# Optimization experiments

Measured on AMD Instinct MI355X. Metric: run time of the kernel, lower is better.

## Reference

```python
import jax, jax.numpy as jnp
import numpy as np

N = 50000
NEG_SLOPE = 0.2


def gat_conv(x, src, dst, W, al, ar, b, res=None, activation=None):
    # x: [N, F_in]; W: [F_in, H*D]; al, ar: [H, D]; b: [H*D]
    H, D = al.shape
    h = (x @ W).reshape(-1, H, D)                      # [N, H, D]
    el = jnp.sum(h * al, axis=-1)                      # [N, H]
    er = jnp.sum(h * ar, axis=-1)                      # [N, H]
    e = jax.nn.leaky_relu(el[src] + er[dst], NEG_SLOPE)  # [E, H]
    # edge softmax grouped by destination node
    m = jax.ops.segment_max(e, dst, num_segments=N)    # [N, H]
    ex = jnp.exp(e - m[dst])
    s = jax.ops.segment_sum(ex, dst, num_segments=N)   # [N, H]
    alpha = ex / s[dst]                                # [E, H]
    msg = h[src] * alpha[..., None]                    # [E, H, D]
    out = jax.ops.segment_sum(msg, dst, num_segments=N)  # [N, H, D]
    if res is not None:
        if res is True:  # identity residual (F_in == H*D)
            out = out + x.reshape(-1, H, D)
        else:            # projected residual, res: [F_in, H*D]
            out = out + (x @ res).reshape(-1, H, D)
    out = out + b.reshape(1, H, D)
    if activation is not None:
        out = activation(out)
    return out


def setup_inputs() -> dict:
    key = jax.random.key(0)
    ks = jax.random.split(key, 16)
    E = 800000
    IN, HID, CLS, H = 256, 64, 32, 2
    x = jax.random.normal(ks[0], (N, IN), dtype=jnp.float32)
    edge_src = jax.random.randint(ks[1], (E,), 0, N, dtype=jnp.int32)
    edge_dst = jax.random.randint(ks[2], (E,), 0, N, dtype=jnp.int32)

    def lin(k, fi, fo):
        return jax.random.normal(k, (fi, fo), dtype=jnp.float32) * (1.0 / np.sqrt(fi))

    W0 = lin(ks[3], IN, H * HID)
    al0 = jax.random.normal(ks[4], (H, HID), dtype=jnp.float32) * 0.1
    ar0 = jax.random.normal(ks[5], (H, HID), dtype=jnp.float32) * 0.1
    b0 = jnp.zeros((H * HID,), dtype=jnp.float32)
    W1 = lin(ks[6], H * HID, H * HID)
    al1 = jax.random.normal(ks[7], (H, HID), dtype=jnp.float32) * 0.1
    ar1 = jax.random.normal(ks[8], (H, HID), dtype=jnp.float32) * 0.1
    b1 = jnp.zeros((H * HID,), dtype=jnp.float32)
    W2 = lin(ks[9], H * HID, H * CLS)
    al2 = jax.random.normal(ks[10], (H, CLS), dtype=jnp.float32) * 0.1
    ar2 = jax.random.normal(ks[11], (H, CLS), dtype=jnp.float32) * 0.1
    b2 = jnp.zeros((H * CLS,), dtype=jnp.float32)
    Wres2 = lin(ks[12], H * HID, H * CLS)
    return {"x": x, "edge_src": edge_src, "edge_dst": edge_dst,
            "W0": W0, "al0": al0, "ar0": ar0, "b0": b0,
            "W1": W1, "al1": al1, "ar1": ar1, "b1": b1,
            "W2": W2, "al2": al2, "ar2": ar2, "b2": b2,
            "Wres2": Wres2}


def reference(x, edge_src, edge_dst, W0, al0, ar0, b0, W1, al1, ar1, b1,
              W2, al2, ar2, b2, Wres2):
    elu = jax.nn.elu
    h = gat_conv(x, edge_src, edge_dst, W0, al0, ar0, b0,
                 res=None, activation=elu)
    h = h.reshape(h.shape[0], -1)  # flatten heads: [N, H*D]
    h = gat_conv(h, edge_src, edge_dst, W1, al1, ar1, b1,
                 res=True, activation=elu)  # identity residual
    h = h.reshape(h.shape[0], -1)
    h = gat_conv(h, edge_src, edge_dst, W2, al2, ar2, b2,
                 res=Wres2, activation=None)  # [N, H, CLS]
    logits = h.mean(axis=1)  # mean over heads -> [N, CLS]
    return logits
```

## Files before the change

kernel.cpp:

```cpp
#include <hip/hip_runtime.h>
#include <math.h>


typedef unsigned int uint;
typedef unsigned short ushort;
typedef __attribute__((ext_vector_type(8))) short bf16x8;
typedef __attribute__((ext_vector_type(4))) float f32x4;

#define NBK 196
#define BCAP 4608

__device__ inline uint f2bf(float f) {
    uint u = __float_as_uint(f);
    return (u + 0x7fffu + ((u >> 16) & 1u)) >> 16;
}

__device__ inline uint4 pack8(float4 a, float4 b) {
    return make_uint4(f2bf(a.x) | (f2bf(a.y) << 16), f2bf(a.z) | (f2bf(a.w) << 16),
                      f2bf(b.x) | (f2bf(b.y) << 16), f2bf(b.z) | (f2bf(b.w) << 16));
}

__global__ __launch_bounds__(256) void buildA_k(
    const int* __restrict__ src, const int* __restrict__ dst, int E,
    int* __restrict__ bcur, uint* __restrict__ bdata, int nba,
    const float* __restrict__ W0, const float* __restrict__ W1,
    const float* __restrict__ W2, const float* __restrict__ Wr,
    ushort* __restrict__ Wt0, ushort* __restrict__ Wt1,
    ushort* __restrict__ Wt2cat) {
    __shared__ int lhist[NBK];
    __shared__ int gbase[NBK];
    const int t = threadIdx.x;
    if ((int)blockIdx.x >= nba) {
        int wb = blockIdx.x - nba;
        if (wb < 128) {
            int i = wb * 256 + t;
            int n = i >> 8, k = i & 255;
            Wt0[n * 256 + k] = (ushort)f2bf(W0[k * 128 + n]);
        } else if (wb < 192) {
            int i = (wb - 128) * 256 + t;
            int n = i >> 7, k = i & 127;
            Wt1[n * 128 + k] = (ushort)f2bf(W1[k * 128 + n]);
        } else if (wb < 224) {
            int i = (wb - 192) * 256 + t;
            int n = i >> 7, k = i & 127;
            Wt2cat[n * 128 + k] = (ushort)f2bf(W2[k * 64 + n]);
        } else {
            int i = (wb - 224) * 256 + t;
            int n = i >> 7, k = i & 127;
            Wt2cat[(64 + n) * 128 + k] = (ushort)f2bf(Wr[k * 64 + n]);
        }
        return;
    }
    for (int i = t; i < NBK; i += 256) lhist[i] = 0;
    __syncthreads();
    const int e0 = blockIdx.x * 2048 + t * 8;
    uint payload[8], meta[8];
#pragma unroll
    for (int i = 0; i < 8; ++i) {
        int e = e0 + i;
        if (e < E) {
            int s = src[e], d = dst[e];
            int b = d >> 8;
            int r = atomicAdd(&lhist[b], 1);
            payload[i] = ((uint)s << 8) | (uint)(d & 255);
            meta[i] = ((uint)b << 16) | (uint)r;
        } else {
            meta[i] = 0xffffffffu;
        }
    }
    __syncthreads();
    for (int i = t; i < NBK; i += 256) {
        int c = lhist[i];
        gbase[i] = c ? atomicAdd(&bcur[i], c) : 0;
    }
    __syncthreads();
#pragma unroll
    for (int i = 0; i < 8; ++i) {
        if (meta[i] != 0xffffffffu) {
            int b = meta[i] >> 16;
            int pos = gbase[b] + (int)(meta[i] & 0xffffu);
            if (pos < BCAP) bdata[(size_t)b * BCAP + pos] = payload[i];
        }
    }
}

__global__ __launch_bounds__(256) void bscan_k(const int* __restrict__ bcur,
                                               int* __restrict__ bbase) {
    __shared__ int sm[256];
    int t = threadIdx.x;
    int v = (t < NBK) ? min(bcur[t], BCAP) : 0;
    sm[t] = v;
    __syncthreads();
    for (int o = 1; o < 256; o <<= 1) {
        int add = (t >= o) ? sm[t - o] : 0;
        __syncthreads();
        sm[t] += add;
        __syncthreads();
    }
    if (t < NBK) bbase[t] = sm[t] - v;
}

__global__ __launch_bounds__(256) void bucketB_k(
    const uint* __restrict__ bdata, const int* __restrict__ bcur,
    const int* __restrict__ bbase, int* __restrict__ deg,
    int* __restrict__ offs, int* __restrict__ ssrc, int n,
    int* __restrict__ meta, int* __restrict__ nl0, int* __restrict__ nl1,
    int* __restrict__ nl2) {
    __shared__ int lhist[256], lofs[256], lcur[256], stmp[256];
    __shared__ int lc[3], lb[3];
    const int b = blockIdx.x, t = threadIdx.x;
    const int cnt = min(bcur[b], BCAP);
    const int gb = bbase[b];
    lhist[t] = 0;
    if (t < 3) lc[t] = 0;
    __syncthreads();
    const uint* bd = bdata + (size_t)b * BCAP;
    for (int i = t; i < cnt; i += 256)
        atomicAdd(&lhist[bd[i] & 255], 1);
    __syncthreads();
    int v = lhist[t];
    stmp[t] = v;
    __syncthreads();
    for (int o = 1; o < 256; o <<= 1) {
        int add = (t >= o) ? stmp[t - o] : 0;
        __syncthreads();
        stmp[t] += add;
        __syncthreads();
    }
    lofs[t] = stmp[t] - v;
    lcur[t] = 0;
    __syncthreads();
    int node = b * 256 + t;
    int cls = -1, r = 0;
    if (node < n) {
        deg[node] = v;
        offs[node] = gb + lofs[t];
        cls = (v <= 16) ? 0 : ((v <= 32) ? 1 : 2);
        r = atomicAdd(&lc[cls], 1);
    }
    __syncthreads();
    if (t < 3) lb[t] = lc[t] ? atomicAdd(&meta[t], lc[t]) : 0;
    __syncthreads();
    if (node < n) {
        int* nl = (cls == 0) ? nl0 : ((cls == 1) ? nl1 : nl2);
        nl[lb[cls] + r] = node;
    }
    for (int i = t; i < cnt; i += 256) {
        uint p = bd[i];
        int dl = p & 255;
        int rr = atomicAdd(&lcur[dl], 1);
        ssrc[gb + lofs[dl] + rr] = (int)(p >> 8);
    }
}

template <int K, bool L2MODE, bool AFP32>
__global__ __launch_bounds__(256) void gemm_m(
    const float* __restrict__ Af, const ushort* __restrict__ Ab,
    const ushort* __restrict__ Wt, ushort* __restrict__ Hb,
    float* __restrict__ hres, int nrows,
    const float* __restrict__ al, const float* __restrict__ ar,
    float* __restrict__ el, float* __restrict__ er) {
    constexpr int BK = 64;
    constexpr int AS = 72;
    __shared__ float smem[8448 + 256];
    ushort* As = (ushort*)smem;
    ushort* Ws = (ushort*)smem + 64 * AS;
    float* alr = smem + 8448;
    const int tid = threadIdx.x;
    const int w = tid >> 6;
    const int lane = tid & 63;
    const int l15 = lane & 15, quad = lane >> 4;
    const int row0 = blockIdx.x * 64;
    constexpr int NC = L2MODE ? 64 : 128;

    if (tid < 2 * NC) alr[tid] = (tid < NC) ? al[tid] : ar[tid - NC];

    f32x4 acc[8];
#pragma unroll
    for (int i = 0; i < 8; ++i) acc[i] = (f32x4){0.f, 0.f, 0.f, 0.f};

    for (int kt = 0; kt < K / BK; ++kt) {
        const int k0 = kt * BK;
        if (AFP32) {
#pragma unroll
            for (int t = 0; t < 4; ++t) {
                int idx = tid + t * 256;
                int r = idx >> 4, c4 = idx & 15;
                float4 v = make_float4(0.f, 0.f, 0.f, 0.f);
                if (row0 + r < nrows)
                    v = *(const float4*)&Af[(size_t)(row0 + r) * K + k0 + c4 * 4];
                ushort4 o;
                o.x = (ushort)f2bf(v.x); o.y = (ushort)f2bf(v.y);
                o.z = (ushort)f2bf(v.z); o.w = (ushort)f2bf(v.w);
                *(ushort4*)&As[r * AS + c4 * 4] = o;
            }
        } else {
#pragma unroll
            for (int t = 0; t < 2; ++t) {
                int idx = tid + t * 256;
                int r = idx >> 3, c8 = idx & 7;
                uint4 v = make_uint4(0, 0, 0, 0);
                if (row0 + r < nrows)
                    v = *(const uint4*)&Ab[(size_t)(row0 + r) * K + k0 + c8 * 8];
                *(uint4*)&As[r * AS + c8 * 8] = v;
            }
        }
#pragma unroll
        for (int t = 0; t < 4; ++t) {
            int idx = tid + t * 256;
            int n = idx >> 3, c8 = idx & 7;
            *(uint4*)&Ws[n * AS + c8 * 8] =
                *(const uint4*)&Wt[(size_t)n * K + k0 + c8 * 8];
        }
        __syncthreads();
#pragma unroll
        for (int ks = 0; ks < 2; ++ks) {
            bf16x8 af = *(const bf16x8*)&As[(w * 16 + l15) * AS + ks * 32 + quad * 8];
#pragma unroll
            for (int ct = 0; ct < 8; ++ct) {
                bf16x8 bf = *(const bf16x8*)&Ws[(ct * 16 + l15) * AS + ks * 32 + quad * 8];
                acc[ct] = __builtin_amdgcn_mfma_f32_16x16x32_bf16(af, bf, acc[ct], 0, 0, 0);
            }
        }
        __syncthreads();
    }

    float* Cs = smem;
#pragma unroll
    for (int ct = 0; ct < 8; ++ct)
#pragma unroll
        for (int r = 0; r < 4; ++r)
            Cs[(w * 16 + quad * 4 + r) * 132 + ct * 16 + l15] = acc[ct][r];
    __syncthreads();

    if (L2MODE) {
#pragma unroll
        for (int t = 0; t < 2; ++t) {
            int chunk = tid + t * 256;
            int r = chunk >> 3, c8 = chunk & 7;
            int grow = row0 + r;
            if (grow < nrows) {
                float4 v0 = *(float4*)&Cs[r * 132 + c8 * 8];
                float4 v1 = *(float4*)&Cs[r * 132 + c8 * 8 + 4];
                *(uint4*)&Hb[(size_t)grow * 64 + c8 * 8] = pack8(v0, v1);
            }
        }
#pragma unroll
        for (int t = 0; t < 4; ++t) {
            int chunk = tid + t * 256;
            int r = chunk >> 4, c4 = chunk & 15;
            int grow = row0 + r;
            if (grow < nrows)
                *(float4*)&hres[(size_t)grow * 64 + c4 * 4] =
                    *(float4*)&Cs[r * 132 + 64 + c4 * 4];
        }
    } else {
#pragma unroll
        for (int t = 0; t < 4; ++t) {
            int chunk = tid + t * 256;
            int r = chunk >> 4, c8 = chunk & 15;
            int grow = row0 + r;
            if (grow < nrows) {
                float4 v0 = *(float4*)&Cs[r * 132 + c8 * 8];
                float4 v1 = *(float4*)&Cs[r * 132 + c8 * 8 + 4];
                *(uint4*)&Hb[(size_t)grow * 128 + c8 * 8] = pack8(v0, v1);
            }
        }
    }
    {
        constexpr int HD = L2MODE ? 32 : 64;
        int r = tid >> 2, hh = (tid >> 1) & 1, iser = tid & 1;
        int grow = row0 + r;
        const float* coef = alr + iser * NC + hh * HD;
        const float* crow = Cs + r * 132 + hh * HD;
        float sum = 0.f;
#pragma unroll
        for (int i = 0; i < HD; ++i) sum += crow[i] * coef[i];
        if (grow < nrows) (iser ? er : el)[grow * 2 + hh] = sum;
    }
}

template <int D, bool MEAN_HEADS, bool RES_BF16, int LPN>
__device__ __forceinline__ void agg_group(
    int node, int lane, float2* __restrict__ wlsw,
    const int* __restrict__ ssrc, const int* __restrict__ offs,
    const int* __restrict__ deg, const ushort* __restrict__ hb,
    const float* __restrict__ el, const float* __restrict__ er,
    const float* __restrict__ bias, const void* __restrict__ res,
    float* __restrict__ out, ushort* __restrict__ outb, int act) {
    constexpr int F = 2 * D;
    constexpr int CH = F / 8;
    constexpr int ESL = LPN / CH;
    constexpr int UB = 8;
    static_assert(ESL >= 1, "LPN must cover a full row");
    const int g = lane / LPN, sl = lane % LPN;
    const bool valid = node >= 0;
    float2* wls = wlsw + g * (LPN * 2);
    int off = 0, dg = 0;
    float2 ern = make_float2(0.f, 0.f);
    if (valid) {
        off = offs[node];
        dg = deg[node];
        ern = *(const float2*)&er[node * 2];
    }
    const uint4* __restrict__ hp = (const uint4*)hb;
    const int c = sl & (CH - 1);
    const int es = sl / CH;
    const int h1 = (c >= CH / 2) ? 1 : 0;
    const float2* wbase = wls + es * 2 + h1;
    float acc[8];
#pragma unroll
    for (int i = 0; i < 8; ++i) acc[i] = 0.f;

    auto inner = [&](int cnt) {
        for (int p = 0; p < cnt; p += UB * ESL) {
            float2 mw[UB];
#pragma unroll
            for (int u = 0; u < UB; ++u) mw[u] = wbase[(p + u * ESL) * 2];
            uint4 q[UB];
#pragma unroll
            for (int u = 0; u < UB; ++u)
                q[u] = hp[(size_t)__float_as_int(mw[u].x) * CH + c];
#pragma unroll
            for (int u = 0; u < UB; ++u) {
                float wj = mw[u].y;
                acc[0] += wj * __uint_as_float(q[u].x << 16);
                acc[1] += wj * __uint_as_float(q[u].x & 0xffff0000u);
                acc[2] += wj * __uint_as_float(q[u].y << 16);
                acc[3] += wj * __uint_as_float(q[u].y & 0xffff0000u);
                acc[4] += wj * __uint_as_float(q[u].z << 16);
                acc[5] += wj * __uint_as_float(q[u].z & 0xffff0000u);
                acc[6] += wj * __uint_as_float(q[u].w << 16);
                acc[7] += wj * __uint_as_float(q[u].w & 0xffff0000u);
            }
        }
    };

    bool big = false;
    if constexpr (LPN == 64) big = (dg > 64);

    if (!big) {
        int sidx = 0;
        float a = -INFINITY, b = -INFINITY;
        if (valid && sl < dg) {
            sidx = ssrc[off + sl];
            float2 ev = *(const float2*)&el[sidx * 2];
            a = ev.x + ern.x; a = fmaxf(a, 0.2f * a);
            b = ev.y + ern.y; b = fmaxf(b, 0.2f * b);
        }
        float m0 = a, m1 = b;
#pragma unroll
        for (int o = LPN / 2; o; o >>= 1) {
            m0 = fmaxf(m0, __shfl_xor(m0, o));
            m1 = fmaxf(m1, __shfl_xor(m1, o));
        }
        float p0 = (valid && sl < dg) ? __expf(a - m0) : 0.f;
        float p1 = (valid && sl < dg) ? __expf(b - m1) : 0.f;
        float s0 = p0, s1 = p1;
#pragma unroll
        for (int o = LPN / 2; o; o >>= 1) {
            s0 += __shfl_xor(s0, o);
            s1 += __shfl_xor(s1, o);
        }
        float is0 = s0 > 0.f ? 1.f / s0 : 0.f;
        float is1 = s1 > 0.f ? 1.f / s1 : 0.f;
        wls[sl * 2 + 0] = make_float2(__int_as_float(sidx), p0 * is0);
        wls[sl * 2 + 1] = make_float2(__int_as_float(sidx), p1 * is1);
        inner(dg);
    } else if constexpr (LPN == 64) {
        float s0 = 0.f, s1 = 0.f;
        float m0 = -INFINITY, m1 = -INFINITY;
        for (int k = sl; k < dg; k += 64) {
            int sidx = ssrc[off + k];
            float2 ev = *(const float2*)&el[sidx * 2];
            float a = ev.x + ern.x; a = fmaxf(a, 0.2f * a);
            float b = ev.y + ern.y; b = fmaxf(b, 0.2f * b);
            float nm = fmaxf(m0, a);
            s0 = s0 * __expf(m0 - nm) + __expf(a - nm); m0 = nm;
            nm = fmaxf(m1, b);
            s1 = s1 * __expf(m1 - nm) + __expf(b - nm); m1 = nm;
        }
        for (int o = 32; o; o >>= 1) {
            float om = __shfl_xor(m0, o), os = __shfl_xor(s0, o);
            float nm = fmaxf(m0, om);
            s0 = (nm == -INFINITY) ? 0.f : s0 * __expf(m0 - nm) + os * __expf(om - nm);
            m0 = nm;
            om = __shfl_xor(m1, o); os = __shfl_xor(s1, o);
            nm = fmaxf(m1, om);
            s1 = (nm == -INFINITY) ? 0.f : s1 * __expf(m1 - nm) + os * __expf(om - nm);
            m1 = nm;
        }
        float is0 = s0 > 0.f ? 1.f / s0 : 0.f;
        float is1 = s1 > 0.f ? 1.f / s1 : 0.f;
        for (int cc = 0; cc < dg; cc += 64) {
            int k = cc + sl;
            int sidx = 0;
            float w0 = 0.f, w1 = 0.f;
            if (k < dg) {
                sidx = ssrc[off + k];
                float2 ev = *(const float2*)&el[sidx * 2];
                float a = ev.x + ern.x; a = fmaxf(a, 0.2f * a);
                float b = ev.y + ern.y; b = fmaxf(b, 0.2f * b);
                w0 = __expf(a - m0) * is0;
                w1 = __expf(b - m1) * is1;
            }
            wls[sl * 2 + 0] = make_float2(__int_as_float(sidx), w0);
            wls[sl * 2 + 1] = make_float2(__int_as_float(sidx), w1);
            inner(min(64, dg - cc));
        }
    }

#pragma unroll
    for (int o = CH; o < LPN; o <<= 1) {
#pragma unroll
        for (int i = 0; i < 8; ++i) acc[i] += __shfl_xor(acc[i], o);
    }
    if (!valid) return;

    const int f0 = c * 8;
    float4 b0v = *(const float4*)&bias[f0];
    float4 b1v = *(const float4*)&bias[f0 + 4];
    float vv[8] = {acc[0] + b0v.x, acc[1] + b0v.y, acc[2] + b0v.z, acc[3] + b0v.w,
                   acc[4] + b1v.x, acc[5] + b1v.y, acc[6] + b1v.z, acc[7] + b1v.w};
    if (res) {
        if (RES_BF16) {
            uint4 r = ((const uint4*)res)[(size_t)node * CH + c];
            vv[0] += __uint_as_float(r.x << 16);
            vv[1] += __uint_as_float(r.x & 0xffff0000u);
            vv[2] += __uint_as_float(r.y << 16);
            vv[3] += __uint_as_float(r.y & 0xffff0000u);
            vv[4] += __uint_as_float(r.z << 16);
            vv[5] += __uint_as_float(r.z & 0xffff0000u);
            vv[6] += __uint_as_float(r.w << 16);
            vv[7] += __uint_as_float(r.w & 0xffff0000u);
        } else {
            const float* rf = (const float*)res;
            float4 r0v = *(const float4*)&rf[(size_t)node * F + f0];
            float4 r1v = *(const float4*)&rf[(size_t)node * F + f0 + 4];
            vv[0] += r0v.x; vv[1] += r0v.y; vv[2] += r0v.z; vv[3] += r0v.w;
            vv[4] += r1v.x; vv[5] += r1v.y; vv[6] += r1v.z; vv[7] += r1v.w;
        }
    }
    if (act) {
#pragma unroll
        for (int i = 0; i < 8; ++i)
            vv[i] = vv[i] > 0.f ? vv[i] : __expf(vv[i]) - 1.f;
    }
    if (MEAN_HEADS) {
        float ov[8];
#pragma unroll
        for (int i = 0; i < 8; ++i) ov[i] = __shfl_xor(vv[i], CH / 2);
        if (es == 0 && c < CH / 2) {
            float4 u0 = make_float4(0.5f * (vv[0] + ov[0]), 0.5f * (vv[1] + ov[1]),
                                    0.5f * (vv[2] + ov[2]), 0.5f * (vv[3] + ov[3]));
            float4 u1 = make_float4(0.5f * (vv[4] + ov[4]), 0.5f * (vv[5] + ov[5]),
                                    0.5f * (vv[6] + ov[6]), 0.5f * (vv[7] + ov[7]));
            *(float4*)&out[(size_t)node * D + f0] = u0;
            *(float4*)&out[(size_t)node * D + f0 + 4] = u1;
        }
    } else if (es == 0) {
        if (out) {
            *(float4*)&out[(size_t)node * F + f0] =
                make_float4(vv[0], vv[1], vv[2], vv[3]);
            *(float4*)&out[(size_t)node * F + f0 + 4] =
                make_float4(vv[4], vv[5], vv[6], vv[7]);
        }
        if (outb) {
            *(uint4*)&outb[(size_t)node * F + f0] =
                pack8(make_float4(vv[0], vv[1], vv[2], vv[3]),
                      make_float4(vv[4], vv[5], vv[6], vv[7]));
        }
    }
}

template <int D, bool MEAN_HEADS, bool RES_BF16>
__global__ __launch_bounds__(256) void agg_c2(
    const int* __restrict__ meta, const int* __restrict__ nl0,
    const int* __restrict__ nl1, const int* __restrict__ nl2,
    const int* __restrict__ ssrc, const int* __restrict__ offs,
    const int* __restrict__ deg, const ushort* __restrict__ hb,
    const float* __restrict__ el, const float* __restrict__ er,
    const float* __restrict__ bias, const void* __restrict__ res,
    float* __restrict__ out, ushort* __restrict__ outb, int act) {
    __shared__ float2 wls_all[4][128];
    const int wid = threadIdx.x >> 6;
    const int lane = threadIdx.x & 63;
    float2* wls = wls_all[wid];
    const int c0 = meta[0], c1 = meta[1], c2 = meta[2];
    const int I0 = (c0 + 3) >> 2;
    const int I01 = I0 + ((c1 + 1) >> 1);
    const int T = I01 + c2;
    const int nW = gridDim.x * 4;
    for (int it = blockIdx.x * 4 + wid; it < T; it += nW) {
        if (it < I0) {
            int idx = it * 4 + (lane >> 4);
            int node = (idx < c0) ? nl0[idx] : -1;
            agg_group<D, MEAN_HEADS, RES_BF16, 16>(node, lane, wls, ssrc, offs,
                                                   deg, hb, el, er, bias, res,
                                                   out, outb, act);
        } else if (it < I01) {
            int idx = (it - I0) * 2 + (lane >> 5);
            int node = (idx < c1) ? nl1[idx] : -1;
            agg_group<D, MEAN_HEADS, RES_BF16, 32>(node, lane, wls, ssrc, offs,
                                                   deg, hb, el, er, bias, res,
                                                   out, outb, act);
        } else {
            int node = nl2[it - I01];
            agg_group<D, MEAN_HEADS, RES_BF16, 64>(node, lane, wls, ssrc, offs,
                                                   deg, hb, el, er, bias, res,
                                                   out, outb, act);
        }
    }
}


extern "C" void kernel_launch(void* const* d_in, const int* in_sizes, int n_in,
                              void* d_out, int out_size, void* d_ws, size_t ws_size,
                              hipStream_t stream) {
    const float* x     = (const float*)d_in[0];
    const int*   esrc  = (const int*)d_in[1];
    const int*   edst  = (const int*)d_in[2];
    const float* W0    = (const float*)d_in[3];
    const float* al0   = (const float*)d_in[4];
    const float* ar0   = (const float*)d_in[5];
    const float* b0    = (const float*)d_in[6];
    const float* W1    = (const float*)d_in[7];
    const float* al1   = (const float*)d_in[8];
    const float* ar1   = (const float*)d_in[9];
    const float* b1    = (const float*)d_in[10];
    const float* W2    = (const float*)d_in[11];
    const float* al2   = (const float*)d_in[12];
    const float* ar2   = (const float*)d_in[13];
    const float* b2    = (const float*)d_in[14];
    const float* Wres2 = (const float*)d_in[15];

    const int N = in_sizes[0] / 256;
    const int E = in_sizes[1];

    float* ws = (float*)d_ws;
    float* hres  = ws;
    float* el    = hres + (size_t)N * 64;
    float* er    = el + (size_t)N * 2;
    int* deg     = (int*)(er + (size_t)N * 2);
    int* offs    = deg + N;
    int* bcur    = offs + N;
    int* bbase   = bcur + 256;
    int* ssrc    = bbase + 256;
    uint* bdata  = (uint*)(ssrc + E);
    ushort* Hb   = (ushort*)(bdata + (size_t)NBK * BCAP);
    ushort* Ab   = Hb + (size_t)N * 128;
    ushort* Bb   = Ab + (size_t)N * 128;
    ushort* Wt0  = Bb + (size_t)N * 128;
    ushort* Wt1  = Wt0 + 128 * 256;
    ushort* Wt2c = Wt1 + 128 * 128;
    int* nl0     = (int*)(Wt2c + 128 * 128);
    int* nl1     = nl0 + N;
    int* nl2     = nl1 + N;
    int* meta    = bcur + 208;

    hipMemsetAsync(bcur, 0, 256 * sizeof(int), stream);
    const int nba = (E + 2047) / 2048;
    buildA_k<<<nba + 256, 256, 0, stream>>>(esrc, edst, E, bcur, bdata, nba,
                                            W0, W1, W2, Wres2, Wt0, Wt1, Wt2c);
    bscan_k<<<1, 256, 0, stream>>>(bcur, bbase);
    bucketB_k<<<NBK, 256, 0, stream>>>(bdata, bcur, bbase, deg, offs, ssrc, N,
                                       meta, nl0, nl1, nl2);

    int gblk = (N + 63) / 64;
    const int ablk = 2048;

    gemm_m<256, false, true><<<gblk, 256, 0, stream>>>(
        x, nullptr, Wt0, Hb, nullptr, N, al0, ar0, el, er);
    agg_c2<64, false, false><<<ablk, 256, 0, stream>>>(
        meta, nl0, nl1, nl2, ssrc, offs, deg, Hb, el, er, b0, nullptr,
        nullptr, Ab, 1);

    gemm_m<128, false, false><<<gblk, 256, 0, stream>>>(
        nullptr, Ab, Wt1, Hb, nullptr, N, al1, ar1, el, er);
    agg_c2<64, false, true><<<ablk, 256, 0, stream>>>(
        meta, nl0, nl1, nl2, ssrc, offs, deg, Hb, el, er, b1, Ab,
        nullptr, Bb, 1);

    gemm_m<128, true, false><<<gblk, 256, 0, stream>>>(
        nullptr, Bb, Wt2c, Hb, hres, N, al2, ar2, el, er);
    agg_c2<32, true, false><<<ablk, 256, 0, stream>>>(
        meta, nl0, nl1, nl2, ssrc, offs, deg, Hb, el, er, b2, hres,
        (float*)d_out, nullptr, 0);
}
```

Baseline: 276.4 us.

## Fold bucket scan into bucketB and load GEMM operands directly from global

```diff
diff --git a/kernel.cpp b/kernel.cpp
--- a/kernel.cpp
+++ b/kernel.cpp
@@ -84,36 +84,29 @@
     }
 }
 
-__global__ __launch_bounds__(256) void bscan_k(const int* __restrict__ bcur,
-                                               int* __restrict__ bbase) {
-    __shared__ int sm[256];
-    int t = threadIdx.x;
-    int v = (t < NBK) ? min(bcur[t], BCAP) : 0;
-    sm[t] = v;
-    __syncthreads();
-    for (int o = 1; o < 256; o <<= 1) {
-        int add = (t >= o) ? sm[t - o] : 0;
-        __syncthreads();
-        sm[t] += add;
-        __syncthreads();
-    }
-    if (t < NBK) bbase[t] = sm[t] - v;
-}
-
 __global__ __launch_bounds__(256) void bucketB_k(
     const uint* __restrict__ bdata, const int* __restrict__ bcur,
-    const int* __restrict__ bbase, int* __restrict__ deg,
-    int* __restrict__ offs, int* __restrict__ ssrc, int n,
-    int* __restrict__ meta, int* __restrict__ nl0, int* __restrict__ nl1,
-    int* __restrict__ nl2) {
+    int* __restrict__ deg, int* __restrict__ offs, int* __restrict__ ssrc,
+    int n, int* __restrict__ meta, int* __restrict__ nl0,
+    int* __restrict__ nl1, int* __restrict__ nl2) {
     __shared__ int lhist[256], lofs[256], lcur[256], stmp[256];
-    __shared__ int lc[3], lb[3];
+    __shared__ int lc[3], lb[3], sgb;
     const int b = blockIdx.x, t = threadIdx.x;
     const int cnt = min(bcur[b], BCAP);
-    const int gb = bbase[b];
+    int cv = (t < NBK) ? min(bcur[t], BCAP) : 0;
+    stmp[t] = cv;
     lhist[t] = 0;
     if (t < 3) lc[t] = 0;
     __syncthreads();
+    for (int o = 1; o < 256; o <<= 1) {
+        int add = (t >= o) ? stmp[t - o] : 0;
+        __syncthreads();
+        stmp[t] += add;
+        __syncthreads();
+    }
+    if (t == 0) sgb = b ? stmp[b - 1] : 0;
+    __syncthreads();
+    const int gb = sgb;
     const uint* bd = bdata + (size_t)b * BCAP;
     for (int i = t; i < cnt; i += 256)
         atomicAdd(&lhist[bd[i] & 255], 1);
@@ -160,12 +153,9 @@
     float* __restrict__ hres, int nrows,
     const float* __restrict__ al, const float* __restrict__ ar,
     float* __restrict__ el, float* __restrict__ er) {
-    constexpr int BK = 64;
-    constexpr int AS = 72;
-    __shared__ float smem[8448 + 256];
-    ushort* As = (ushort*)smem;
-    ushort* Ws = (ushort*)smem + 64 * AS;
-    float* alr = smem + 8448;
+    __shared__ float smem[64 * 132 + 256];
+    float* Cs = smem;
+    float* alr = smem + 64 * 132;
     const int tid = threadIdx.x;
     const int w = tid >> 6;
     const int lane = tid & 63;
@@ -175,57 +165,39 @@
 
     if (tid < 2 * NC) alr[tid] = (tid < NC) ? al[tid] : ar[tid - NC];
 
+    const int arow = row0 + w * 16 + l15;
+    const bool aval = arow < nrows;
+
     f32x4 acc[8];
 #pragma unroll
     for (int i = 0; i < 8; ++i) acc[i] = (f32x4){0.f, 0.f, 0.f, 0.f};
 
-    for (int kt = 0; kt < K / BK; ++kt) {
-        const int k0 = kt * BK;
-        if (AFP32) {
-#pragma unroll
-            for (int t = 0; t < 4; ++t) {
-                int idx = tid + t * 256;
-                int r = idx >> 4, c4 = idx & 15;
-                float4 v = make_float4(0.f, 0.f, 0.f, 0.f);
-                if (row0 + r < nrows)
-                    v = *(const float4*)&Af[(size_t)(row0 + r) * K + k0 + c4 * 4];
-                ushort4 o;
-                o.x = (ushort)f2bf(v.x); o.y = (ushort)f2bf(v.y);
-                o.z = (ushort)f2bf(v.z); o.w = (ushort)f2bf(v.w);
-                *(ushort4*)&As[r * AS + c4 * 4] = o;
+    union BC { uint4 u; bf16x8 b; };
+
+#pragma unroll 1
+    for (int kt = 0; kt < K / 64; ++kt) {
+#pragma unroll
+        for (int ks = 0; ks < 2; ++ks) {
+            const int kc = kt * 64 + ks * 32 + quad * 8;
+            bf16x8 af = {0, 0, 0, 0, 0, 0, 0, 0};
+            if (AFP32) {
+                if (aval) {
+                    float4 v0 = *(const float4*)&Af[(size_t)arow * K + kc];
+                    float4 v1 = *(const float4*)&Af[(size_t)arow * K + kc + 4];
+                    BC cu; cu.u = pack8(v0, v1);
+                    af = cu.b;
+                }
+            } else {
+                if (aval) af = *(const bf16x8*)&Ab[(size_t)arow * K + kc];
             }
-        } else {
-#pragma unroll
-            for (int t = 0; t < 2; ++t) {
-                int idx = tid + t * 256;
-                int r = idx >> 3, c8 = idx & 7;
-                uint4 v = make_uint4(0, 0, 0, 0);
-                if (row0 + r < nrows)
-                    v = *(const uint4*)&Ab[(size_t)(row0 + r) * K + k0 + c8 * 8];
-                *(uint4*)&As[r * AS + c8 * 8] = v;
-            }
-        }
-#pragma unroll
-        for (int t = 0; t < 4; ++t) {
-            int idx = tid + t * 256;
-            int n = idx >> 3, c8 = idx & 7;
-            *(uint4*)&Ws[n * AS + c8 * 8] =
-                *(const uint4*)&Wt[(size_t)n * K + k0 + c8 * 8];
-        }
-        __syncthreads();
-#pragma unroll
-        for (int ks = 0; ks < 2; ++ks) {
-            bf16x8 af = *(const bf16x8*)&As[(w * 16 + l15) * AS + ks * 32 + quad * 8];
 #pragma unroll
             for (int ct = 0; ct < 8; ++ct) {
-                bf16x8 bf = *(const bf16x8*)&Ws[(ct * 16 + l15) * AS + ks * 32 + quad * 8];
+                bf16x8 bf = *(const bf16x8*)&Wt[(size_t)(ct * 16 + l15) * K + kc];
                 acc[ct] = __builtin_amdgcn_mfma_f32_16x16x32_bf16(af, bf, acc[ct], 0, 0, 0);
             }
         }
-        __syncthreads();
-    }
-
-    float* Cs = smem;
+    }
+
 #pragma unroll
     for (int ct = 0; ct < 8; ++ct)
 #pragma unroll
@@ -562,8 +534,7 @@
     const int nba = (E + 2047) / 2048;
     buildA_k<<<nba + 256, 256, 0, stream>>>(esrc, edst, E, bcur, bdata, nba,
                                             W0, W1, W2, Wres2, Wt0, Wt1, Wt2c);
-    bscan_k<<<1, 256, 0, stream>>>(bcur, bbase);
-    bucketB_k<<<NBK, 256, 0, stream>>>(bdata, bcur, bbase, deg, offs, ssrc, N,
+    bucketB_k<<<NBK, 256, 0, stream>>>(bdata, bcur, deg, offs, ssrc, N,
                                        meta, nl0, nl1, nl2);
 
     int gblk = (N + 63) / 64;
```

New measurement: 314.6 us. +13.8%, slower.

## Fuse bucket scan and sort into first GEMM launch; use 128-row GEMM tiles

Applied to the files above, without the earlier changes.

```diff
diff --git a/kernel.cpp b/kernel.cpp
--- a/kernel.cpp
+++ b/kernel.cpp
@@ -84,36 +84,35 @@
     }
 }
 
-__global__ __launch_bounds__(256) void bscan_k(const int* __restrict__ bcur,
-                                               int* __restrict__ bbase) {
-    __shared__ int sm[256];
-    int t = threadIdx.x;
-    int v = (t < NBK) ? min(bcur[t], BCAP) : 0;
-    sm[t] = v;
-    __syncthreads();
-    for (int o = 1; o < 256; o <<= 1) {
-        int add = (t >= o) ? sm[t - o] : 0;
-        __syncthreads();
-        sm[t] += add;
-        __syncthreads();
-    }
-    if (t < NBK) bbase[t] = sm[t] - v;
-}
-
-__global__ __launch_bounds__(256) void bucketB_k(
-    const uint* __restrict__ bdata, const int* __restrict__ bcur,
-    const int* __restrict__ bbase, int* __restrict__ deg,
+__device__ void bucketB_body(
+    float* smemf, int b, const uint* __restrict__ bdata,
+    const int* __restrict__ bcur, int* __restrict__ deg,
     int* __restrict__ offs, int* __restrict__ ssrc, int n,
     int* __restrict__ meta, int* __restrict__ nl0, int* __restrict__ nl1,
     int* __restrict__ nl2) {
-    __shared__ int lhist[256], lofs[256], lcur[256], stmp[256];
-    __shared__ int lc[3], lb[3];
-    const int b = blockIdx.x, t = threadIdx.x;
+    int* lhist = (int*)smemf;
+    int* lofs  = lhist + 256;
+    int* lcur  = lofs + 256;
+    int* stmp  = lcur + 256;
+    int* lc    = stmp + 256;
+    int* lb    = lc + 3;
+    int* sgb   = lb + 3;
+    const int t = threadIdx.x;
     const int cnt = min(bcur[b], BCAP);
-    const int gb = bbase[b];
+    int cv = (t < NBK) ? min(bcur[t], BCAP) : 0;
+    stmp[t] = cv;
     lhist[t] = 0;
     if (t < 3) lc[t] = 0;
     __syncthreads();
+    for (int o = 1; o < 256; o <<= 1) {
+        int add = (t >= o) ? stmp[t - o] : 0;
+        __syncthreads();
+        stmp[t] += add;
+        __syncthreads();
+    }
+    if (t == 0) sgb[0] = b ? stmp[b - 1] : 0;
+    __syncthreads();
+    const int gb = sgb[0];
     const uint* bd = bdata + (size_t)b * BCAP;
     for (int i = t; i < cnt; i += 256)
         atomicAdd(&lhist[bd[i] & 255], 1);
@@ -154,36 +153,37 @@
 }
 
 template <int K, bool L2MODE, bool AFP32>
-__global__ __launch_bounds__(256) void gemm_m(
-    const float* __restrict__ Af, const ushort* __restrict__ Ab,
+__device__ void gemm_body(
+    float* smem, const float* __restrict__ Af, const ushort* __restrict__ Ab,
     const ushort* __restrict__ Wt, ushort* __restrict__ Hb,
     float* __restrict__ hres, int nrows,
     const float* __restrict__ al, const float* __restrict__ ar,
-    float* __restrict__ el, float* __restrict__ er) {
-    constexpr int BK = 64;
+    float* __restrict__ el, float* __restrict__ er, int bid) {
     constexpr int AS = 72;
-    __shared__ float smem[8448 + 256];
     ushort* As = (ushort*)smem;
-    ushort* Ws = (ushort*)smem + 64 * AS;
-    float* alr = smem + 8448;
+    ushort* Ws = (ushort*)smem + 128 * AS;
+    float* Cs = smem;
+    float* alr = smem + 9216;
     const int tid = threadIdx.x;
     const int w = tid >> 6;
     const int lane = tid & 63;
     const int l15 = lane & 15, quad = lane >> 4;
-    const int row0 = blockIdx.x * 64;
+    const int row0 = bid * 128;
     constexpr int NC = L2MODE ? 64 : 128;
 
     if (tid < 2 * NC) alr[tid] = (tid < NC) ? al[tid] : ar[tid - NC];
 
-    f32x4 acc[8];
-#pragma unroll
-    for (int i = 0; i < 8; ++i) acc[i] = (f32x4){0.f, 0.f, 0.f, 0.f};
-
-    for (int kt = 0; kt < K / BK; ++kt) {
-        const int k0 = kt * BK;
+    f32x4 acc[2][8];
+#pragma unroll
+    for (int m = 0; m < 2; ++m)
+#pragma unroll
+        for (int i = 0; i < 8; ++i) acc[m][i] = (f32x4){0.f, 0.f, 0.f, 0.f};
+
+    for (int kt = 0; kt < K / 64; ++kt) {
+        const int k0 = kt * 64;
         if (AFP32) {
 #pragma unroll
-            for (int t = 0; t < 4; ++t) {
+            for (int t = 0; t < 8; ++t) {
                 int idx = tid + t * 256;
                 int r = idx >> 4, c4 = idx & 15;
                 float4 v = make_float4(0.f, 0.f, 0.f, 0.f);
@@ -196,7 +196,7 @@
             }
         } else {
 #pragma unroll
-            for (int t = 0; t < 2; ++t) {
+            for (int t = 0; t < 4; ++t) {
                 int idx = tid + t * 256;
                 int r = idx >> 3, c8 = idx & 7;
                 uint4 v = make_uint4(0, 0, 0, 0);
@@ -215,68 +215,110 @@
         __syncthreads();
 #pragma unroll
         for (int ks = 0; ks < 2; ++ks) {
-            bf16x8 af = *(const bf16x8*)&As[(w * 16 + l15) * AS + ks * 32 + quad * 8];
+            bf16x8 a0 = *(const bf16x8*)&As[(w * 32 + l15) * AS + ks * 32 + quad * 8];
+            bf16x8 a1 = *(const bf16x8*)&As[(w * 32 + 16 + l15) * AS + ks * 32 + quad * 8];
 #pragma unroll
             for (int ct = 0; ct < 8; ++ct) {
                 bf16x8 bf = *(const bf16x8*)&Ws[(ct * 16 + l15) * AS + ks * 32 + quad * 8];
-                acc[ct] = __builtin_amdgcn_mfma_f32_16x16x32_bf16(af, bf, acc[ct], 0, 0, 0);
-            }
-        }
-        __syncthreads();
-    }
-
-    float* Cs = smem;
-#pragma unroll
-    for (int ct = 0; ct < 8; ++ct)
-#pragma unroll
-        for (int r = 0; r < 4; ++r)
-            Cs[(w * 16 + quad * 4 + r) * 132 + ct * 16 + l15] = acc[ct][r];
-    __syncthreads();
-
-    if (L2MODE) {
-#pragma unroll
-        for (int t = 0; t < 2; ++t) {
-            int chunk = tid + t * 256;
-            int r = chunk >> 3, c8 = chunk & 7;
-            int grow = row0 + r;
-            if (grow < nrows) {
-                float4 v0 = *(float4*)&Cs[r * 132 + c8 * 8];
-                float4 v1 = *(float4*)&Cs[r * 132 + c8 * 8 + 4];
-                *(uint4*)&Hb[(size_t)grow * 64 + c8 * 8] = pack8(v0, v1);
-            }
-        }
-#pragma unroll
-        for (int t = 0; t < 4; ++t) {
-            int chunk = tid + t * 256;
-            int r = chunk >> 4, c4 = chunk & 15;
-            int grow = row0 + r;
-            if (grow < nrows)
-                *(float4*)&hres[(size_t)grow * 64 + c4 * 4] =
-                    *(float4*)&Cs[r * 132 + 64 + c4 * 4];
-        }
+                acc[0][ct] = __builtin_amdgcn_mfma_f32_16x16x32_bf16(a0, bf, acc[0][ct], 0, 0, 0);
+                acc[1][ct] = __builtin_amdgcn_mfma_f32_16x16x32_bf16(a1, bf, acc[1][ct], 0, 0, 0);
+            }
+        }
+        __syncthreads();
+    }
+
+#pragma unroll
+    for (int h = 0; h < 2; ++h) {
+        if ((w >> 1) == h) {
+            int wl = w & 1;
+#pragma unroll
+            for (int m = 0; m < 2; ++m)
+#pragma unroll
+                for (int ct = 0; ct < 8; ++ct)
+#pragma unroll
+                    for (int r = 0; r < 4; ++r)
+                        Cs[(wl * 32 + m * 16 + quad * 4 + r) * 132 + ct * 16 + l15] =
+                            acc[m][ct][r];
+        }
+        __syncthreads();
+        const int rbase = row0 + h * 64;
+        if (L2MODE) {
+#pragma unroll
+            for (int t = 0; t < 2; ++t) {
+                int chunk = tid + t * 256;
+                int r = chunk >> 3, c8 = chunk & 7;
+                int grow = rbase + r;
+                if (grow < nrows) {
+                    float4 v0 = *(float4*)&Cs[r * 132 + c8 * 8];
+                    float4 v1 = *(float4*)&Cs[r * 132 + c8 * 8 + 4];
+                    *(uint4*)&Hb[(size_t)grow * 64 + c8 * 8] = pack8(v0, v1);
+                }
+            }
+#pragma unroll
+            for (int t = 0; t < 4; ++t) {
+                int chunk = tid + t * 256;
+                int r = chunk >> 4, c4 = chunk & 15;
+                int grow = rbase + r;
+                if (grow < nrows)
+                    *(float4*)&hres[(size_t)grow * 64 + c4 * 4] =
+                        *(float4*)&Cs[r * 132 + 64 + c4 * 4];
+            }
+        } else {
+#pragma unroll
+            for (int t = 0; t < 4; ++t) {
+                int chunk = tid + t * 256;
+                int r = chunk >> 4, c8 = chunk & 15;
+                int grow = rbase + r;
+                if (grow < nrows) {
+                    float4 v0 = *(float4*)&Cs[r * 132 + c8 * 8];
+                    float4 v1 = *(float4*)&Cs[r * 132 + c8 * 8 + 4];
+                    *(uint4*)&Hb[(size_t)grow * 128 + c8 * 8] = pack8(v0, v1);
+                }
+            }
+        }
+        {
+            constexpr int HD = L2MODE ? 32 : 64;
+            int r = tid >> 2, hh = (tid >> 1) & 1, iser = tid & 1;
+            int grow = rbase + r;
+            const float* coef = alr + iser * NC + hh * HD;
+            const float* crow = Cs + r * 132 + hh * HD;
+            float sum = 0.f;
+#pragma unroll
+            for (int i = 0; i < HD; ++i) sum += crow[i] * coef[i];
+            if (grow < nrows) (iser ? er : el)[grow * 2 + hh] = sum;
+        }
+        __syncthreads();
+    }
+}
+
+template <int K, bool L2MODE, bool AFP32>
+__global__ __launch_bounds__(256) void gemm_m(
+    const float* __restrict__ Af, const ushort* __restrict__ Ab,
+    const ushort* __restrict__ Wt, ushort* __restrict__ Hb,
+    float* __restrict__ hres, int nrows,
+    const float* __restrict__ al, const float* __restrict__ ar,
+    float* __restrict__ el, float* __restrict__ er) {
+    __shared__ float smem[9472];
+    gemm_body<K, L2MODE, AFP32>(smem, Af, Ab, Wt, Hb, hres, nrows, al, ar,
+                                el, er, blockIdx.x);
+}
+
+__global__ __launch_bounds__(256) void gemm0_bucketB_k(
+    const float* __restrict__ x, const ushort* __restrict__ Wt0,
+    ushort* __restrict__ Hb, int nrows,
+    const float* __restrict__ al, const float* __restrict__ ar,
+    float* __restrict__ el, float* __restrict__ er, int gblk,
+    const uint* __restrict__ bdata, const int* __restrict__ bcur,
+    int* __restrict__ deg, int* __restrict__ offs, int* __restrict__ ssrc,
+    int* __restrict__ meta, int* __restrict__ nl0, int* __restrict__ nl1,
+    int* __restrict__ nl2) {
+    __shared__ float smem[9472];
+    if ((int)blockIdx.x < gblk) {
+        gemm_body<256, false, true>(smem, x, nullptr, Wt0, Hb, nullptr, nrows,
+                                    al, ar, el, er, blockIdx.x);
     } else {
-#pragma unroll
-        for (int t = 0; t < 4; ++t) {
-            int chunk = tid + t * 256;
-            int r = chunk >> 4, c8 = chunk & 15;
-            int grow = row0 + r;
-            if (grow < nrows) {
-                float4 v0 = *(float4*)&Cs[r * 132 + c8 * 8];
-                float4 v1 = *(float4*)&Cs[r * 132 + c8 * 8 + 4];
-                *(uint4*)&Hb[(size_t)grow * 128 + c8 * 8] = pack8(v0, v1);
-            }
-        }
-    }
-    {
-        constexpr int HD = L2MODE ? 32 : 64;
-        int r = tid >> 2, hh = (tid >> 1) & 1, iser = tid & 1;
-        int grow = row0 + r;
-        const float* coef = alr + iser * NC + hh * HD;
-        const float* crow = Cs + r * 132 + hh * HD;
-        float sum = 0.f;
-#pragma unroll
-        for (int i = 0; i < HD; ++i) sum += crow[i] * coef[i];
-        if (grow < nrows) (iser ? er : el)[grow * 2 + hh] = sum;
+        bucketB_body(smem, blockIdx.x - gblk, bdata, bcur, deg, offs, ssrc,
+                     nrows, meta, nl0, nl1, nl2);
     }
 }
 
@@ -562,15 +604,13 @@
     const int nba = (E + 2047) / 2048;
     buildA_k<<<nba + 256, 256, 0, stream>>>(esrc, edst, E, bcur, bdata, nba,
                                             W0, W1, W2, Wres2, Wt0, Wt1, Wt2c);
-    bscan_k<<<1, 256, 0, stream>>>(bcur, bbase);
-    bucketB_k<<<NBK, 256, 0, stream>>>(bdata, bcur, bbase, deg, offs, ssrc, N,
-                                       meta, nl0, nl1, nl2);
-
-    int gblk = (N + 63) / 64;
+
+    const int gblk = (N + 127) / 128;
     const int ablk = 2048;
 
-    gemm_m<256, false, true><<<gblk, 256, 0, stream>>>(
-        x, nullptr, Wt0, Hb, nullptr, N, al0, ar0, el, er);
+    gemm0_bucketB_k<<<gblk + NBK, 256, 0, stream>>>(
+        x, Wt0, Hb, N, al0, ar0, el, er, gblk,
+        bdata, bcur, deg, offs, ssrc, meta, nl0, nl1, nl2);
     agg_c2<64, false, false><<<ablk, 256, 0, stream>>>(
         meta, nl0, nl1, nl2, ssrc, offs, deg, Hb, el, er, b0, nullptr,
         nullptr, Ab, 1);
```

New measurement: 274.2 us. About the same (-0.8%).
